# Optimization experiments

Measured on AMD Instinct MI355X. Metric: run time of the kernel, lower is better.

## Reference

```python
import jax, jax.numpy as jnp
import numpy as np

D_MODEL = 1024
NHEAD = 16
D_K = D_MODEL // NHEAD
B, S = 4, 2048
LN_EPS = 1e-5


def setup_inputs() -> dict:
    key = jax.random.key(0)
    ks = jax.random.split(key, 12)
    sd = 1.0 / np.sqrt(D_MODEL)
    inp = {
        'x': jax.random.normal(ks[0], (B, S, D_MODEL), dtype=jnp.float32),
        'wq': jax.random.normal(ks[1], (D_MODEL, D_MODEL), dtype=jnp.float32) * sd,
        'bq': jnp.zeros((D_MODEL,), dtype=jnp.float32),
        'wk': jax.random.normal(ks[2], (D_MODEL, D_MODEL), dtype=jnp.float32) * sd,
        'bk': jnp.zeros((D_MODEL,), dtype=jnp.float32),
        'wv': jax.random.normal(ks[3], (D_MODEL, D_MODEL), dtype=jnp.float32) * sd,
        'bv': jnp.zeros((D_MODEL,), dtype=jnp.float32),
        'wo': jax.random.normal(ks[4], (D_MODEL, D_MODEL), dtype=jnp.float32) * sd,
        'bo': jnp.zeros((D_MODEL,), dtype=jnp.float32),
        'conv_w': jax.random.normal(ks[5], (D_MODEL, 3), dtype=jnp.float32) * (1.0 / np.sqrt(3.0)),
        'conv_b': jnp.zeros((D_MODEL,), dtype=jnp.float32),
        'ln_g': jnp.ones((D_MODEL,), dtype=jnp.float32),
        'ln_b': jnp.zeros((D_MODEL,), dtype=jnp.float32),
    }
    return inp


def _forward(x, wq, bq, wk, bk, wv, bv, wo, bo, conv_w, conv_b, ln_g, ln_b):
    b, s, d = x.shape
    # QKV projections -> [B, H, S, Dk]
    q = (x @ wq.T + bq).reshape(b, s, NHEAD, D_K).transpose(0, 2, 1, 3)
    k = (x @ wk.T + bk).reshape(b, s, NHEAD, D_K).transpose(0, 2, 1, 3)
    v = (x @ wv.T + bv).reshape(b, s, NHEAD, D_K).transpose(0, 2, 1, 3)
    # full attention, materialized scores [B, H, S, S]
    scores = jnp.einsum('bhqd,bhkd->bhqk', q, k) / jnp.sqrt(jnp.float32(D_K))
    attn = jax.nn.softmax(scores, axis=-1)  # dropout is identity in eval
    ctx = jnp.einsum('bhqk,bhkd->bhqd', attn, v)
    ctx = ctx.transpose(0, 2, 1, 3).reshape(b, s, d)
    global_attn = ctx @ wo.T + bo
    # depthwise conv1d, kernel 3, padding 1 along sequence
    xp = jnp.pad(x, ((0, 0), (1, 1), (0, 0)))
    local_attn = (xp[:, :-2] * conv_w[:, 0]
                  + xp[:, 1:-1] * conv_w[:, 1]
                  + xp[:, 2:] * conv_w[:, 2]
                  + conv_b)
    combined = global_attn + 0.3 * local_attn
    y = x + combined  # dropout identity in eval
    mu = jnp.mean(y, axis=-1, keepdims=True)
    var = jnp.mean(jnp.square(y - mu), axis=-1, keepdims=True)
    return (y - mu) * jax.lax.rsqrt(var + LN_EPS) * ln_g + ln_b


def reference(x, wq, bq, wk, bk, wv, bv, wo, bo, conv_w, conv_b, ln_g, ln_b):
    return _forward(x, wq, bq, wk, bk, wv, bv, wo, bo, conv_w, conv_b, ln_g, ln_b)
```

## Files before the change

### kernel.cpp

```cpp
#include <hip/hip_runtime.h>

#define DEV __device__ __forceinline__

typedef unsigned short u16;
typedef unsigned int u32;
using f32x4  = __attribute__((ext_vector_type(4))) float;
using f32x16 = __attribute__((ext_vector_type(16))) float;
using s16x8  = __attribute__((ext_vector_type(8))) short;
using u32x2  = __attribute__((ext_vector_type(2))) u32;
using u32x4  = __attribute__((ext_vector_type(4))) u32;
typedef int i32x2 __attribute__((ext_vector_type(2)));

#if __has_builtin(__builtin_amdgcn_exp2f)
#define EXP2(x) __builtin_amdgcn_exp2f(x)
#else
#define EXP2(x) exp2f(x)
#endif

DEV u16 f2b(float f) {
  union { float f; u32 u; } v; v.f = f;
  return (u16)((v.u + 0x7FFFu + ((v.u >> 16) & 1u)) >> 16);
}
DEV float b2f(u16 u) {
  union { u32 u; float f; } v; v.u = ((u32)u) << 16;
  return v.f;
}

DEV u32 cvtpk(float lo, float hi) {
  u32 r;
  asm("v_cvt_pk_bf16_f32 %0, %1, %2" : "=v"(r) : "v"(lo), "v"(hi));
  return r;
}

#if __has_builtin(__builtin_amdgcn_permlane32_swap)
DEV void lane32_swap(u32& x, u32& y) {
  i32x2 r = __builtin_amdgcn_permlane32_swap((int)x, (int)y, false, false);
  x = (u32)r[0]; y = (u32)r[1];
}
#else
DEV void lane32_swap(u32& x, u32& y) {
  u32 xo = (u32)__shfl_xor((int)x, 32, 64);
  u32 yo = (u32)__shfl_xor((int)y, 32, 64);
  int hi = (int)((threadIdx.x & 63) >> 5);
  u32 nx = hi ? yo : x;
  u32 ny = hi ? y : xo;
  x = nx; y = ny;
}
#endif

DEV void gload16(const void* g, void* l) {
  __builtin_amdgcn_global_load_lds(
      (const __attribute__((address_space(1))) void*)g,
      (__attribute__((address_space(3))) void*)l, 16, 0, 0);
}

__global__ __launch_bounds__(256) void k_cvt(const float* __restrict__ src,
                                             u16* __restrict__ dst, int n4) {
  int i = blockIdx.x * 256 + threadIdx.x;
  if (i >= n4) return;
  float4 v = ((const float4*)src)[i];
  ushort4 o;
  o.x = f2b(v.x); o.y = f2b(v.y); o.z = f2b(v.z); o.w = f2b(v.w);
  ((ushort4*)dst)[i] = o;
}

template <bool RB>
__global__ __launch_bounds__(256) void k_gemm_bt(
    const u16* __restrict__ A, const u16* __restrict__ Bw,
    const float* __restrict__ bias, u16* __restrict__ C,
    int M, int N, int K) {
  __shared__ alignas(16) u16 lds_[16384];
  char* lds = (char*)lds_;
  const int t = threadIdx.x;
  const int wave = t >> 6, lane = t & 63;
  const int g = lane >> 4, fr = lane & 15;
  const int wr = (wave >> 1) * 64, wc = (wave & 1) * 64;
  const int m0 = blockIdx.y * 128, n0 = blockIdx.x * 128;
  const int chunk = t & 3;

  auto stage = [&](int k0, int buf) {
#pragma unroll
    for (int r = 0; r < 2; ++r) {
      int row = r * 64 + (t >> 2);
      int sw = 8 * (chunk ^ ((row >> 1) & 3));
      char* dst = lds + buf * 16384 + r * 4096 + wave * 1024;
      gload16(A  + (size_t)(m0 + row) * K + k0 + sw, dst);
      gload16(Bw + (size_t)(n0 + row) * K + k0 + sw, dst + 8192);
    }
  };

  f32x4 acc[4][4];
#pragma unroll
  for (int i = 0; i < 4; ++i)
#pragma unroll
    for (int j = 0; j < 4; ++j)
#pragma unroll
      for (int r = 0; r < 4; ++r) acc[i][j][r] = 0.f;

  const int nk = K >> 5;
  stage(0, 0);
  __syncthreads();
  for (int kt = 0; kt < nk; ++kt) {
    const int cur = kt & 1;
    if (kt + 1 < nk) stage((kt + 1) << 5, cur ^ 1);
    s16x8 af[4], bf4[4];
#pragma unroll
    for (int i = 0; i < 4; ++i) {
      int row = wr + i * 16 + fr;
      af[i] = *(const s16x8*)(lds + cur * 16384 + row * 64 +
                              ((g * 16) ^ ((((row >> 1) & 3)) << 4)));
    }
#pragma unroll
    for (int j = 0; j < 4; ++j) {
      int row = wc + j * 16 + fr;
      bf4[j] = *(const s16x8*)(lds + cur * 16384 + 8192 + row * 64 +
                               ((g * 16) ^ ((((row >> 1) & 3)) << 4)));
    }
#pragma unroll
    for (int i = 0; i < 4; ++i)
#pragma unroll
      for (int j = 0; j < 4; ++j)
        acc[i][j] = __builtin_amdgcn_mfma_f32_16x16x32_bf16(af[i], bf4[j], acc[i][j], 0, 0, 0);
    __syncthreads();
  }
#pragma unroll
  for (int i = 0; i < 4; ++i)
#pragma unroll
    for (int j = 0; j < 4; ++j)
#pragma unroll
      for (int r = 0; r < 4; ++r) {
        int row = m0 + wr + i * 16 + g * 4 + r;
        int col = n0 + wc + j * 16 + fr;
        float v = acc[i][j][r] + (RB ? bias[row] : bias[col]);
        C[(size_t)row * N + col] = f2b(v);
      }
}

__global__ __launch_bounds__(256) void k_attn(
    const u16* __restrict__ qb, const u16* __restrict__ kb,
    const u16* __restrict__ vtb, u16* __restrict__ ctx) {
  __shared__ alignas(16) u16 smem_[16384];
  char* smem = (char*)smem_;
  const int bh = blockIdx.x;
  const int b = bh >> 4, h = bh & 15;
  const int qblk = blockIdx.y;
  const int t = threadIdx.x, w = t >> 6, lane = t & 63;
  const int l31 = lane & 31, hi = lane >> 5;
  const int hc = h * 64;
  const int q0 = qblk * 128 + w * 32;
  const int lrow = lane >> 3, seg = lane & 7;
  const float c2 = 0.18033688011112042f;
  const float S2 = 17.312340490667560f;

  s16x8 qf[4];
  {
    const u16* qrow = qb + (size_t)(b * 2048 + q0 + l31) * 1024 + hc + hi * 8;
#pragma unroll
    for (int ks = 0; ks < 4; ++ks) qf[ks] = *(const s16x8*)(qrow + ks * 16);
  }

  const u16* kbase  = kb  + (size_t)(b * 2048) * 1024 + hc;
  const u16* vtbase = vtb + (size_t)(h * 64) * 8192 + b * 2048;

  auto stage = [&](int kt, int buf) {
    const int k0 = kt * 64;
#pragma unroll
    for (int r = 0; r < 2; ++r) {
      int row = r * 32 + w * 8 + lrow;
      int sw = 8 * (seg ^ (row & 7));
      char* dst = smem + buf * 16384 + r * 4096 + w * 1024;
      gload16(kbase  + (size_t)(k0 + row) * 1024 + sw, dst);
      gload16(vtbase + (size_t)row * 8192 + k0 + sw, dst + 8192);
    }
  };

  f32x16 octx[2];
#pragma unroll
  for (int dt = 0; dt < 2; ++dt)
#pragma unroll
    for (int r = 0; r < 16; ++r) octx[dt][r] = 0.f;
  float l_run = 0.f;

  stage(0, 0);
  __syncthreads();
  for (int kt = 0; kt < 32; ++kt) {
    const int cur = kt & 1;
    if (kt + 1 < 32) stage(kt + 1, cur ^ 1);

    f32x16 st[2];
#pragma unroll
    for (int tt = 0; tt < 2; ++tt)
#pragma unroll
      for (int r = 0; r < 16; ++r) st[tt][r] = 0.f;
#pragma unroll
    for (int ks = 0; ks < 4; ++ks)
#pragma unroll
      for (int tt = 0; tt < 2; ++tt) {
        int row = tt * 32 + l31;
        s16x8 kf = *(const s16x8*)(smem + cur * 16384 + row * 128 +
                                   ((ks * 32 + hi * 16) ^ ((row & 7) << 4)));
        st[tt] = __builtin_amdgcn_mfma_f32_32x32x16_bf16(kf, qf[ks], st[tt], 0, 0, 0);
      }

    float sm = 0.f;
#pragma unroll
    for (int tt = 0; tt < 2; ++tt)
#pragma unroll
      for (int r = 0; r < 16; ++r) {
        float p = EXP2(__builtin_fmaf(st[tt][r], c2, -S2));
        st[tt][r] = p;
        sm += p;
      }
    l_run += sm;

    u32 pw[2][8];
#pragma unroll
    for (int tt = 0; tt < 2; ++tt)
#pragma unroll
      for (int p = 0; p < 8; ++p) pw[tt][p] = cvtpk(st[tt][2 * p], st[tt][2 * p + 1]);
    s16x8 pf[4];
#pragma unroll
    for (int ks = 0; ks < 4; ++ks) {
      int tt = ks >> 1, kp = (ks & 1) * 4;
      u32 u0 = pw[tt][kp + 0], v0 = pw[tt][kp + 2];
      u32 u1 = pw[tt][kp + 1], v1 = pw[tt][kp + 3];
      lane32_swap(u0, v0);
      lane32_swap(u1, v1);
      u32x4 f; f[0] = u0; f[1] = u1; f[2] = v0; f[3] = v1;
      pf[ks] = __builtin_bit_cast(s16x8, f);
    }

#pragma unroll
    for (int dt = 0; dt < 2; ++dt)
#pragma unroll
      for (int ks = 0; ks < 4; ++ks) {
        int row = dt * 32 + l31;
        s16x8 vf = *(const s16x8*)(smem + cur * 16384 + 8192 + row * 128 +
                                   ((ks * 32 + hi * 16) ^ ((row & 7) << 4)));
        octx[dt] = __builtin_amdgcn_mfma_f32_32x32x16_bf16(vf, pf[ks], octx[dt], 0, 0, 0);
      }
    __syncthreads();
  }

  {
    u32 ua = __builtin_bit_cast(u32, l_run), va = ua;
    lane32_swap(ua, va);
    l_run = __builtin_bit_cast(float, ua) + __builtin_bit_cast(float, va);
  }
  const float linv = 1.0f / l_run;

  const int ql = w * 32 + l31;
#pragma unroll
  for (int dt = 0; dt < 2; ++dt)
#pragma unroll
    for (int rq = 0; rq < 4; ++rq) {
      int d0 = 8 * rq + 4 * hi + 32 * dt;
      u32x2 pk;
      pk[0] = cvtpk(octx[dt][4 * rq + 0] * linv, octx[dt][4 * rq + 1] * linv);
      pk[1] = cvtpk(octx[dt][4 * rq + 2] * linv, octx[dt][4 * rq + 3] * linv);
      *(u32x2*)(smem + ql * 128 + ((2 * d0) ^ ((ql & 7) << 4))) = pk;
    }
  __syncthreads();
  {
    int qr = t >> 1, half = t & 1;
    u16* dst = ctx + (size_t)(b * 2048 + qblk * 128 + qr) * 1024 + hc + half * 32;
#pragma unroll
    for (int i = 0; i < 4; ++i) {
      s16x8 v = *(const s16x8*)(smem + qr * 128 +
                                ((half * 64 + i * 16) ^ ((qr & 7) << 4)));
      *(s16x8*)(dst + i * 8) = v;
    }
  }
}

__global__ __launch_bounds__(256) void k_epi(
    const float* __restrict__ x, const u16* __restrict__ gab,
    const float* __restrict__ cw, const float* __restrict__ cb,
    const float* __restrict__ lg, const float* __restrict__ lb,
    float* __restrict__ out) {
  __shared__ float red[4];
  const int n = blockIdx.x;
  const int s = n & 2047;
  const int t = threadIdx.x;
  const int d0 = t * 4;
  const float* xr = x + (size_t)n * 1024;

  float xc[4], xm[4], xp[4];
  { float4 v = *(const float4*)(xr + d0); xc[0]=v.x; xc[1]=v.y; xc[2]=v.z; xc[3]=v.w; }
  if (s > 0) { float4 v = *(const float4*)(xr - 1024 + d0); xm[0]=v.x; xm[1]=v.y; xm[2]=v.z; xm[3]=v.w; }
  else { xm[0]=xm[1]=xm[2]=xm[3]=0.f; }
  if (s < 2047) { float4 v = *(const float4*)(xr + 1024 + d0); xp[0]=v.x; xp[1]=v.y; xp[2]=v.z; xp[3]=v.w; }
  else { xp[0]=xp[1]=xp[2]=xp[3]=0.f; }
  ushort4 gv = *(const ushort4*)(gab + (size_t)n * 1024 + d0);
  float ga4[4] = { b2f(gv.x), b2f(gv.y), b2f(gv.z), b2f(gv.w) };

  float y[4];
#pragma unroll
  for (int i = 0; i < 4; ++i) {
    int d = d0 + i;
    float lo = xm[i] * cw[d * 3] + xc[i] * cw[d * 3 + 1] + xp[i] * cw[d * 3 + 2] + cb[d];
    y[i] = xc[i] + ga4[i] + 0.3f * lo;
  }

  float sm = y[0] + y[1] + y[2] + y[3];
#pragma unroll
  for (int off = 32; off >= 1; off >>= 1) sm += __shfl_xor(sm, off, 64);
  if ((t & 63) == 0) red[t >> 6] = sm;
  __syncthreads();
  float mu = (red[0] + red[1] + red[2] + red[3]) * (1.f / 1024.f);
  __syncthreads();

  float vs = 0.f;
#pragma unroll
  for (int i = 0; i < 4; ++i) { float dd = y[i] - mu; vs += dd * dd; }
#pragma unroll
  for (int off = 32; off >= 1; off >>= 1) vs += __shfl_xor(vs, off, 64);
  if ((t & 63) == 0) red[t >> 6] = vs;
  __syncthreads();
  float var = (red[0] + red[1] + red[2] + red[3]) * (1.f / 1024.f);
  float rs = rsqrtf(var + 1e-5f);
#pragma unroll
  for (int i = 0; i < 4; ++i) {
    int d = d0 + i;
    out[(size_t)n * 1024 + d] = (y[i] - mu) * rs * lg[d] + lb[d];
  }
}

extern "C" void kernel_launch(void* const* d_in, const int* in_sizes, int n_in,
                              void* d_out, int out_size, void* d_ws, size_t ws_size,
                              hipStream_t stream) {
  const float* x  = (const float*)d_in[0];
  const float* wq = (const float*)d_in[1];
  const float* bq = (const float*)d_in[2];
  const float* wk = (const float*)d_in[3];
  const float* bk = (const float*)d_in[4];
  const float* wv = (const float*)d_in[5];
  const float* bv = (const float*)d_in[6];
  const float* wo = (const float*)d_in[7];
  const float* bo = (const float*)d_in[8];
  const float* cw = (const float*)d_in[9];
  const float* cb = (const float*)d_in[10];
  const float* lg = (const float*)d_in[11];
  const float* lb = (const float*)d_in[12];
  float* out = (float*)d_out;

  char* ws = (char*)d_ws;
  const size_t MB = 1ull << 20;
  u16* xb  = (u16*)(ws + 0);
  u16* wqb = (u16*)(ws + 16 * MB);
  u16* wkb = (u16*)(ws + 18 * MB);
  u16* wvb = (u16*)(ws + 20 * MB);
  u16* wob = (u16*)(ws + 22 * MB);
  u16* qb  = (u16*)(ws + 24 * MB);
  u16* kb  = (u16*)(ws + 40 * MB);
  u16* vtb = (u16*)(ws + 56 * MB);
  u16* ctx = xb;
  u16* gab = qb;

  k_cvt<<<8192, 256, 0, stream>>>(x, xb, 2097152);
  k_cvt<<<1024, 256, 0, stream>>>(wq, wqb, 262144);
  k_cvt<<<1024, 256, 0, stream>>>(wk, wkb, 262144);
  k_cvt<<<1024, 256, 0, stream>>>(wv, wvb, 262144);
  k_cvt<<<1024, 256, 0, stream>>>(wo, wob, 262144);

  k_gemm_bt<false><<<dim3(8, 64), 256, 0, stream>>>(xb, wqb, bq, qb, 8192, 1024, 1024);
  k_gemm_bt<false><<<dim3(8, 64), 256, 0, stream>>>(xb, wkb, bk, kb, 8192, 1024, 1024);
  k_gemm_bt<true ><<<dim3(64, 8), 256, 0, stream>>>(wvb, xb, bv, vtb, 1024, 8192, 1024);

  k_attn<<<dim3(64, 16), 256, 0, stream>>>(qb, kb, vtb, ctx);

  k_gemm_bt<false><<<dim3(8, 64), 256, 0, stream>>>(ctx, wob, bo, gab, 8192, 1024, 1024);

  k_epi<<<8192, 256, 0, stream>>>(x, gab, cw, cb, lg, lb, out);
}
```

Measured before the change: 241.1 us.

## Fuse Q/K projections, fold softmax scale into K, MFMA row-sum, setprio

The Q and K projections now run as a single GEMM with N=2048, relying on the contiguous wq/wk bf16 buffers, and write one interleaved QK buffer. The K half is pre-scaled by the log2-softmax constant in the GEMM epilogue. The score MFMA chain is seeded with the -S2 shift, so the attention loop no longer needs a per-element FMA or accumulator zeroing. The softmax denominator is now computed by an extra MFMA against a ones vector instead of scalar adds and a lane swap, and s_setprio is raised around the MFMA blocks. The trade-off is extra MFMA work per tile and bf16 rounding of the scaled K values.

Result: faster. 223.9 us (-7.2%).

```diff
diff --git a/kernel.cpp b/kernel.cpp
--- a/kernel.cpp
+++ b/kernel.cpp
@@ -17,6 +17,9 @@
 #define EXP2(x) exp2f(x)
 #endif
 
+__constant__ const float C2_SCALE = 0.18033688011112042f;
+#define S2_SHIFT 17.312340490667560f
+
 DEV u16 f2b(float f) {
   union { float f; u32 u; } v; v.f = f;
   return (u16)((v.u + 0x7FFFu + ((v.u >> 16) & 1u)) >> 16);
@@ -64,11 +67,11 @@
   ((ushort4*)dst)[i] = o;
 }
 
-template <bool RB>
+template <int MODE>
 __global__ __launch_bounds__(256) void k_gemm_bt(
     const u16* __restrict__ A, const u16* __restrict__ Bw,
-    const float* __restrict__ bias, u16* __restrict__ C,
-    int M, int N, int K) {
+    const float* __restrict__ bias0, const float* __restrict__ bias1,
+    u16* __restrict__ C, int M, int N, int K) {
   __shared__ alignas(16) u16 lds_[16384];
   char* lds = (char*)lds_;
   const int t = threadIdx.x;
@@ -116,29 +119,40 @@
       bf4[j] = *(const s16x8*)(lds + cur * 16384 + 8192 + row * 64 +
                                ((g * 16) ^ ((((row >> 1) & 3)) << 4)));
     }
+    __builtin_amdgcn_s_setprio(1);
 #pragma unroll
     for (int i = 0; i < 4; ++i)
 #pragma unroll
       for (int j = 0; j < 4; ++j)
         acc[i][j] = __builtin_amdgcn_mfma_f32_16x16x32_bf16(af[i], bf4[j], acc[i][j], 0, 0, 0);
+    __builtin_amdgcn_s_setprio(0);
     __syncthreads();
   }
 #pragma unroll
-  for (int i = 0; i < 4; ++i)
-#pragma unroll
-    for (int j = 0; j < 4; ++j)
+  for (int j = 0; j < 4; ++j) {
+    const int coltile = n0 + wc + j * 16;
+    float sc = 1.f;
+    const float* bp = bias0;
+    if constexpr (MODE == 2) {
+      if (coltile >= 1024) { bp = bias1 - 1024; sc = C2_SCALE; }
+    }
+#pragma unroll
+    for (int i = 0; i < 4; ++i)
 #pragma unroll
       for (int r = 0; r < 4; ++r) {
         int row = m0 + wr + i * 16 + g * 4 + r;
-        int col = n0 + wc + j * 16 + fr;
-        float v = acc[i][j][r] + (RB ? bias[row] : bias[col]);
+        int col = coltile + fr;
+        float v;
+        if constexpr (MODE == 1) v = acc[i][j][r] + bias0[row];
+        else                     v = (acc[i][j][r] + bp[col]) * sc;
         C[(size_t)row * N + col] = f2b(v);
       }
+  }
 }
 
 __global__ __launch_bounds__(256) void k_attn(
-    const u16* __restrict__ qb, const u16* __restrict__ kb,
-    const u16* __restrict__ vtb, u16* __restrict__ ctx) {
+    const u16* __restrict__ qkb, const u16* __restrict__ vtb,
+    u16* __restrict__ ctx) {
   __shared__ alignas(16) u16 smem_[16384];
   char* smem = (char*)smem_;
   const int bh = blockIdx.x;
@@ -149,18 +163,16 @@
   const int hc = h * 64;
   const int q0 = qblk * 128 + w * 32;
   const int lrow = lane >> 3, seg = lane & 7;
-  const float c2 = 0.18033688011112042f;
-  const float S2 = 17.312340490667560f;
 
   s16x8 qf[4];
   {
-    const u16* qrow = qb + (size_t)(b * 2048 + q0 + l31) * 1024 + hc + hi * 8;
+    const u16* qrow = qkb + (size_t)(b * 2048 + q0 + l31) * 2048 + hc + hi * 8;
 #pragma unroll
     for (int ks = 0; ks < 4; ++ks) qf[ks] = *(const s16x8*)(qrow + ks * 16);
   }
 
-  const u16* kbase  = kb  + (size_t)(b * 2048) * 1024 + hc;
-  const u16* vtbase = vtb + (size_t)(h * 64) * 8192 + b * 2048;
+  const u16* kbase  = qkb + (size_t)(b * 2048) * 2048 + 1024 + hc;
+  const u16* vtbase = vtb + (size_t)hc * 8192 + b * 2048;
 
   auto stage = [&](int kt, int buf) {
     const int k0 = kt * 64;
@@ -169,17 +181,19 @@
       int row = r * 32 + w * 8 + lrow;
       int sw = 8 * (seg ^ (row & 7));
       char* dst = smem + buf * 16384 + r * 4096 + w * 1024;
-      gload16(kbase  + (size_t)(k0 + row) * 1024 + sw, dst);
+      gload16(kbase  + (size_t)(k0 + row) * 2048 + sw, dst);
       gload16(vtbase + (size_t)row * 8192 + k0 + sw, dst + 8192);
     }
   };
 
-  f32x16 octx[2];
-#pragma unroll
-  for (int dt = 0; dt < 2; ++dt)
-#pragma unroll
-    for (int r = 0; r < 16; ++r) octx[dt][r] = 0.f;
-  float l_run = 0.f;
+  f32x16 octx[2], lacc, ns2;
+#pragma unroll
+  for (int r = 0; r < 16; ++r) {
+    octx[0][r] = 0.f; octx[1][r] = 0.f; lacc[r] = 0.f; ns2[r] = -S2_SHIFT;
+  }
+  s16x8 ones;
+#pragma unroll
+  for (int j = 0; j < 8; ++j) ones[j] = (short)0x3F80;
 
   stage(0, 0);
   __syncthreads();
@@ -188,10 +202,7 @@
     if (kt + 1 < 32) stage(kt + 1, cur ^ 1);
 
     f32x16 st[2];
-#pragma unroll
-    for (int tt = 0; tt < 2; ++tt)
-#pragma unroll
-      for (int r = 0; r < 16; ++r) st[tt][r] = 0.f;
+    __builtin_amdgcn_s_setprio(1);
 #pragma unroll
     for (int ks = 0; ks < 4; ++ks)
 #pragma unroll
@@ -199,25 +210,18 @@
         int row = tt * 32 + l31;
         s16x8 kf = *(const s16x8*)(smem + cur * 16384 + row * 128 +
                                    ((ks * 32 + hi * 16) ^ ((row & 7) << 4)));
-        st[tt] = __builtin_amdgcn_mfma_f32_32x32x16_bf16(kf, qf[ks], st[tt], 0, 0, 0);
+        st[tt] = __builtin_amdgcn_mfma_f32_32x32x16_bf16(
+            kf, qf[ks], ks == 0 ? ns2 : st[tt], 0, 0, 0);
       }
-
-    float sm = 0.f;
+    __builtin_amdgcn_s_setprio(0);
+
+    u32 pw[2][8];
 #pragma unroll
     for (int tt = 0; tt < 2; ++tt)
 #pragma unroll
-      for (int r = 0; r < 16; ++r) {
-        float p = EXP2(__builtin_fmaf(st[tt][r], c2, -S2));
-        st[tt][r] = p;
-        sm += p;
-      }
-    l_run += sm;
-
-    u32 pw[2][8];
-#pragma unroll
-    for (int tt = 0; tt < 2; ++tt)
-#pragma unroll
-      for (int p = 0; p < 8; ++p) pw[tt][p] = cvtpk(st[tt][2 * p], st[tt][2 * p + 1]);
+      for (int p = 0; p < 8; ++p)
+        pw[tt][p] = cvtpk(EXP2(st[tt][2 * p]), EXP2(st[tt][2 * p + 1]));
+
     s16x8 pf[4];
 #pragma unroll
     for (int ks = 0; ks < 4; ++ks) {
@@ -230,6 +234,7 @@
       pf[ks] = __builtin_bit_cast(s16x8, f);
     }
 
+    __builtin_amdgcn_s_setprio(1);
 #pragma unroll
     for (int dt = 0; dt < 2; ++dt)
 #pragma unroll
@@ -239,15 +244,14 @@
                                    ((ks * 32 + hi * 16) ^ ((row & 7) << 4)));
         octx[dt] = __builtin_amdgcn_mfma_f32_32x32x16_bf16(vf, pf[ks], octx[dt], 0, 0, 0);
       }
+#pragma unroll
+    for (int ks = 0; ks < 4; ++ks)
+      lacc = __builtin_amdgcn_mfma_f32_32x32x16_bf16(ones, pf[ks], lacc, 0, 0, 0);
+    __builtin_amdgcn_s_setprio(0);
     __syncthreads();
   }
 
-  {
-    u32 ua = __builtin_bit_cast(u32, l_run), va = ua;
-    lane32_swap(ua, va);
-    l_run = __builtin_bit_cast(float, ua) + __builtin_bit_cast(float, va);
-  }
-  const float linv = 1.0f / l_run;
+  const float linv = 1.0f / lacc[0];
 
   const int ql = w * 32 + l31;
 #pragma unroll
@@ -351,11 +355,10 @@
   u16* wkb = (u16*)(ws + 18 * MB);
   u16* wvb = (u16*)(ws + 20 * MB);
   u16* wob = (u16*)(ws + 22 * MB);
-  u16* qb  = (u16*)(ws + 24 * MB);
-  u16* kb  = (u16*)(ws + 40 * MB);
+  u16* qkb = (u16*)(ws + 24 * MB);
   u16* vtb = (u16*)(ws + 56 * MB);
   u16* ctx = xb;
-  u16* gab = qb;
+  u16* gab = qkb;
 
   k_cvt<<<8192, 256, 0, stream>>>(x, xb, 2097152);
   k_cvt<<<1024, 256, 0, stream>>>(wq, wqb, 262144);
@@ -363,13 +366,12 @@
   k_cvt<<<1024, 256, 0, stream>>>(wv, wvb, 262144);
   k_cvt<<<1024, 256, 0, stream>>>(wo, wob, 262144);
 
-  k_gemm_bt<false><<<dim3(8, 64), 256, 0, stream>>>(xb, wqb, bq, qb, 8192, 1024, 1024);
-  k_gemm_bt<false><<<dim3(8, 64), 256, 0, stream>>>(xb, wkb, bk, kb, 8192, 1024, 1024);
-  k_gemm_bt<true ><<<dim3(64, 8), 256, 0, stream>>>(wvb, xb, bv, vtb, 1024, 8192, 1024);
-
-  k_attn<<<dim3(64, 16), 256, 0, stream>>>(qb, kb, vtb, ctx);
-
-  k_gemm_bt<false><<<dim3(8, 64), 256, 0, stream>>>(ctx, wob, bo, gab, 8192, 1024, 1024);
+  k_gemm_bt<2><<<dim3(16, 64), 256, 0, stream>>>(xb, wqb, bq, bk, qkb, 8192, 2048, 1024);
+  k_gemm_bt<1><<<dim3(64, 8), 256, 0, stream>>>(wvb, xb, bv, nullptr, vtb, 1024, 8192, 1024);
+
+  k_attn<<<dim3(64, 16), 256, 0, stream>>>(qkb, vtb, ctx);
+
+  k_gemm_bt<0><<<dim3(8, 64), 256, 0, stream>>>(ctx, wob, bo, nullptr, gab, 8192, 1024, 1024);
 
   k_epi<<<8192, 256, 0, stream>>>(x, gab, cw, cb, lg, lb, out);
 }
```
